# Optimization experiments

Hardware: AMD Instinct MI355X
Metric: run time of the kernel (lower is better)

The kernel has to match this reference:

```python
import jax, jax.numpy as jnp
import numpy as np

B, S, H = 32, 2048, 1024

def setup_inputs() -> dict:
    key = jax.random.key(0)
    ks = jax.random.split(key, 8)
    scale = 1.0 / np.sqrt(H)
    return {
        "query": jax.random.normal(ks[0], (B, H), jnp.float32),
        "keys": jax.random.normal(ks[1], (B, S, H), jnp.float32),
        "Wa_w": jax.random.uniform(ks[2], (H, H), jnp.float32, -scale, scale),
        "Wa_b": jax.random.uniform(ks[3], (H,), jnp.float32, -scale, scale),
        "Ua_w": jax.random.uniform(ks[4], (H, H), jnp.float32, -scale, scale),
        "Ua_b": jax.random.uniform(ks[5], (H,), jnp.float32, -scale, scale),
        "Va_w": jax.random.uniform(ks[6], (1, H), jnp.float32, -scale, scale),
        "Va_b": jax.random.uniform(ks[7], (1,), jnp.float32, -scale, scale),
    }

def reference(query, keys, Wa_w, Wa_b, Ua_w, Ua_b, Va_w, Va_b):
    # q_proj: [B, H]; k_proj: [B, S, H]  (torch Linear: x @ W^T + b)
    q_proj = query @ Wa_w.T + Wa_b
    k_proj = jnp.einsum("bsh,gh->bsg", keys, Ua_w) + Ua_b
    # scores: [B, S, 1] via thin Va projection of tanh-combined features
    scores = jnp.tanh(q_proj[:, None, :] + k_proj) @ Va_w.T + Va_b
    weights = jax.nn.softmax(scores, axis=1)            # [B, S, 1]
    context = jnp.einsum("bsx,bsh->bxh", weights, keys)  # [B, 1, H]
    return context, weights[:, :, 0]
```

## Files before the change

### kernel.cpp

```cpp
#include <hip/hip_runtime.h>
#include <hip/hip_bf16.h>
#include <stdint.h>

#define B_ 32
#define S_ 2048
#define H_ 1024

typedef __attribute__((ext_vector_type(8))) short short8;
typedef __attribute__((ext_vector_type(4))) float floatx4;

__device__ inline unsigned short f32_bf16(float f) {
    union { float f; unsigned u; } v; v.f = f;
    unsigned u = v.u;
    u += 0x7fff + ((u >> 16) & 1);
    return (unsigned short)(u >> 16);
}
__device__ inline unsigned pack_bf2(float a, float b) {
    return (unsigned)f32_bf16(a) | ((unsigned)f32_bf16(b) << 16);
}
__device__ inline float bf_lo(unsigned u) { union { unsigned u; float f; } v; v.u = u << 16; return v.f; }
__device__ inline float bf_hi(unsigned u) { union { unsigned u; float f; } v; v.u = u & 0xffff0000u; return v.f; }

__device__ inline float tanh_fast(float x) {
    float e = __expf(2.0f * x);
    return 1.0f - 2.0f / (e + 1.0f);
}

__device__ inline void gld16(const void* g, void* l) {
    __builtin_amdgcn_global_load_lds(
        (const __attribute__((address_space(1))) unsigned int*)g,
        (__attribute__((address_space(3))) unsigned int*)l, 16, 0, 0);
}

#define KCVT_BLOCKS 32768
#define UACVT_BLOCKS 512
#define QP_BLOCKS 64
__global__ void k_prep(const float* __restrict__ keys, unsigned short* __restrict__ keysbf,
                       const float* __restrict__ ua, unsigned short* __restrict__ uab,
                       const float* __restrict__ query, const float* __restrict__ Wa_w,
                       const float* __restrict__ Wa_b, const float* __restrict__ Ua_b,
                       float* __restrict__ qsum) {
    int blk = blockIdx.x, t = threadIdx.x;
    if (blk < KCVT_BLOCKS + UACVT_BLOCKS) {
        const float* src; unsigned short* dst; size_t base;
        if (blk < KCVT_BLOCKS) { src = keys; dst = keysbf; base = (size_t)blk * 2048; }
        else { src = ua; dst = uab; base = (size_t)(blk - KCVT_BLOCKS) * 2048; }
        float4 v0 = *(const float4*)(src + base + t * 4);
        float4 v1 = *(const float4*)(src + base + 1024 + t * 4);
        *(uint2*)(dst + base + t * 4)        = make_uint2(pack_bf2(v0.x, v0.y), pack_bf2(v0.z, v0.w));
        *(uint2*)(dst + base + 1024 + t * 4) = make_uint2(pack_bf2(v1.x, v1.y), pack_bf2(v1.z, v1.w));
    } else {
        __shared__ float qs_l[32][68];
        int g0 = (blk - KCVT_BLOCKS - UACVT_BLOCKS) * 16;
        int r = t >> 4, l = t & 15;
        int g = g0 + r;
        float acc[32];
#pragma unroll
        for (int b = 0; b < 32; ++b) acc[b] = 0.0f;
        int sb = t >> 3, sc = (t & 7) * 8;
        for (int hc = 0; hc < 16; ++hc) {
            __syncthreads();
            float4 v0 = *(const float4*)(query + (size_t)sb * H_ + hc * 64 + sc);
            float4 v1 = *(const float4*)(query + (size_t)sb * H_ + hc * 64 + sc + 4);
            *(float4*)&qs_l[sb][sc]     = v0;
            *(float4*)&qs_l[sb][sc + 4] = v1;
            __syncthreads();
            float4 w = *(const float4*)(Wa_w + (size_t)g * H_ + hc * 64 + l * 4);
#pragma unroll
            for (int b = 0; b < 32; ++b) {
                float4 q4 = *(const float4*)&qs_l[b][l * 4];
                acc[b] += w.x * q4.x + w.y * q4.y + w.z * q4.z + w.w * q4.w;
            }
        }
#pragma unroll
        for (int b = 0; b < 32; ++b) {
            float a = acc[b];
            a += __shfl_xor(a, 1); a += __shfl_xor(a, 2);
            a += __shfl_xor(a, 4); a += __shfl_xor(a, 8);
            acc[b] = a;
        }
        if (l == 0) {
            float bias = Wa_b[g] + Ua_b[g];
#pragma unroll
            for (int b = 0; b < 32; ++b) qsum[b * H_ + g] = acc[b] + bias;
        }
    }
}

#define BM 128
#define BN 128
#define BK 64

__global__ __launch_bounds__(256, 4) void k_scores(
    const unsigned short* __restrict__ keysbf, const unsigned short* __restrict__ uab,
    const float* __restrict__ qsum, const float* __restrict__ va,
    float* __restrict__ scores_p)
{
    __shared__ unsigned short Al[BM * BK];
    __shared__ unsigned short Bl[BN * BK];

    int bx = blockIdx.x;
    int x  = bx & 7;
    int i  = bx >> 3;
    int tile_m = x * 64 + (i >> 3);
    int nc     = i & 7;
    int m_base = tile_m * BM;
    int b      = m_base >> 11;
    int g0     = nc * BN;

    int tid = threadIdx.x;
    int wid = tid >> 6, lane = tid & 63;
    int wm = wid >> 1, wn = wid & 1;
    int q = lane >> 4, cn = lane & 15;

    int rl8 = lane >> 3;
    int gcg = (lane & 7) ^ rl8;
    const unsigned short* pA[4];
    const unsigned short* pB[4];
    unsigned short* lA[4];
    unsigned short* lB[4];
#pragma unroll
    for (int j = 0; j < 4; ++j) {
        int row = wid * 32 + j * 8 + rl8;
        pA[j] = keysbf + (size_t)(m_base + row) * H_ + gcg * 8;
        pB[j] = uab    + (size_t)(g0     + row) * H_ + gcg * 8;
        lA[j] = &Al[(wid * 32 + j * 8) * BK];
        lB[j] = &Bl[(wid * 32 + j * 8) * BK];
    }

    int aoff[2][4], boff[2][4];
#pragma unroll
    for (int kk = 0; kk < 2; ++kk)
#pragma unroll
        for (int ii = 0; ii < 4; ++ii) {
            int r  = wm * 64 + ii * 16 + cn;
            aoff[kk][ii] = r * BK + ((kk * 4 + q) ^ (r & 7)) * 8;
            int rb = wn * 64 + ii * 16 + cn;
            boff[kk][ii] = rb * BK + ((kk * 4 + q) ^ (rb & 7)) * 8;
        }

    floatx4 acc[4][4];
#pragma unroll
    for (int ii = 0; ii < 4; ++ii)
#pragma unroll
        for (int jj = 0; jj < 4; ++jj)
            acc[ii][jj] = (floatx4)(0.0f);

    for (int kc = 0; kc < H_ / BK; ++kc) {
        __syncthreads();
        int ko = kc * BK;
#pragma unroll
        for (int j = 0; j < 4; ++j) {
            gld16(pA[j] + ko, lA[j]);
            gld16(pB[j] + ko, lB[j]);
        }
        __syncthreads();
#pragma unroll
        for (int kk = 0; kk < 2; ++kk) {
            short8 af[4], bf[4];
#pragma unroll
            for (int ii = 0; ii < 4; ++ii) af[ii] = *(const short8*)&Al[aoff[kk][ii]];
#pragma unroll
            for (int jj = 0; jj < 4; ++jj) bf[jj] = *(const short8*)&Bl[boff[kk][jj]];
#pragma unroll
            for (int ii = 0; ii < 4; ++ii)
#pragma unroll
                for (int jj = 0; jj < 4; ++jj)
                    acc[ii][jj] = __builtin_amdgcn_mfma_f32_16x16x32_bf16(
                        af[ii], bf[jj], acc[ii][jj], 0, 0, 0);
        }
    }

    float qs[4], vw[4];
#pragma unroll
    for (int jj = 0; jj < 4; ++jj) {
        int g = g0 + wn * 64 + jj * 16 + cn;
        qs[jj] = qsum[b * H_ + g];
        vw[jj] = va[g];
    }
    float* slab = scores_p + (size_t)nc * (B_ * S_) + b * S_;
#pragma unroll
    for (int ii = 0; ii < 4; ++ii) {
        float rs[4] = {0.f, 0.f, 0.f, 0.f};
#pragma unroll
        for (int jj = 0; jj < 4; ++jj) {
#pragma unroll
            for (int r = 0; r < 4; ++r)
                rs[r] += vw[jj] * tanh_fast(qs[jj] + acc[ii][jj][r]);
        }
#pragma unroll
        for (int r = 0; r < 4; ++r) {
            for (int mm = 1; mm < 16; mm <<= 1)
                rs[r] += __shfl_xor(rs[r], mm);
        }
        if (cn == 0) {
            int msrow = (m_base & (S_ - 1)) + wm * 64 + ii * 16 + q * 4;
            float* sp = slab + (size_t)wn * (8 * B_ * S_) + msrow;
            sp[0] = rs[0]; sp[1] = rs[1]; sp[2] = rs[2]; sp[3] = rs[3];
        }
    }
}

__global__ void k_softmax(const float* __restrict__ scores_p, float* __restrict__ weights) {
    int b = blockIdx.x;
    int t = threadIdx.x;
    __shared__ float red[4];
    float v[8];
    float mx = -1e30f;
#pragma unroll
    for (int k = 0; k < 8; ++k) {
        int idx = b * S_ + t + k * 256;
        float s = 0.0f;
#pragma unroll
        for (int p = 0; p < 16; ++p) s += scores_p[(size_t)p * (B_ * S_) + idx];
        v[k] = s; mx = fmaxf(mx, s);
    }
    for (int mm = 1; mm < 64; mm <<= 1) mx = fmaxf(mx, __shfl_xor(mx, mm));
    if ((t & 63) == 0) red[t >> 6] = mx;
    __syncthreads();
    mx = fmaxf(fmaxf(red[0], red[1]), fmaxf(red[2], red[3]));
    float sum = 0.0f;
#pragma unroll
    for (int k = 0; k < 8; ++k) { v[k] = __expf(v[k] - mx); sum += v[k]; }
    for (int mm = 1; mm < 64; mm <<= 1) sum += __shfl_xor(sum, mm);
    __syncthreads();
    if ((t & 63) == 0) red[t >> 6] = sum;
    __syncthreads();
    sum = red[0] + red[1] + red[2] + red[3];
    float inv = 1.0f / sum;
#pragma unroll
    for (int k = 0; k < 8; ++k) weights[b * S_ + t + k * 256] = v[k] * inv;
}

__global__ void k_ctx1(const unsigned short* __restrict__ keysbf,
                       const float* __restrict__ weights, float* __restrict__ partial) {
    int blk = blockIdx.x;
    int b = blk >> 5, sc = blk & 31;
    int t = threadIdx.x;
    __shared__ float wl[64];
    if (t < 64) wl[t] = weights[b * S_ + sc * 64 + t];
    __syncthreads();
    const uint4* kp = (const uint4*)(keysbf + (size_t)(b * S_ + sc * 64) * H_);
    int col = t & 127;
    int rp  = t >> 7;
    float a0=0,a1=0,a2=0,a3=0,a4=0,a5=0,a6=0,a7=0;
#pragma unroll 8
    for (int s = rp; s < 64; s += 2) {
        uint4 v = kp[(size_t)s * 128 + col];
        float w = wl[s];
        a0 += w * bf_lo(v.x); a1 += w * bf_hi(v.x);
        a2 += w * bf_lo(v.y); a3 += w * bf_hi(v.y);
        a4 += w * bf_lo(v.z); a5 += w * bf_hi(v.z);
        a6 += w * bf_lo(v.w); a7 += w * bf_hi(v.w);
    }
    float* pp = partial + (size_t)(b * 64 + sc * 2 + rp) * H_ + col * 8;
    float4 o0 = {a0, a1, a2, a3}, o1 = {a4, a5, a6, a7};
    *(float4*)pp = o0;
    *(float4*)(pp + 4) = o1;
}

__global__ void k_ctx2(const float* __restrict__ partial, float* __restrict__ ctx) {
    int b = blockIdx.x;
    int t = threadIdx.x;
    float4 a = {0.f, 0.f, 0.f, 0.f};
#pragma unroll 8
    for (int j = 0; j < 64; ++j) {
        float4 p = *(const float4*)(partial + (size_t)(b * 64 + j) * H_ + t * 4);
        a.x += p.x; a.y += p.y; a.z += p.z; a.w += p.w;
    }
    *(float4*)(ctx + b * H_ + t * 4) = a;
}

extern "C" void kernel_launch(void* const* d_in, const int* in_sizes, int n_in,
                              void* d_out, int out_size, void* d_ws, size_t ws_size,
                              hipStream_t stream) {
    const float* query = (const float*)d_in[0];
    const float* keys  = (const float*)d_in[1];
    const float* Wa_w  = (const float*)d_in[2];
    const float* Wa_b  = (const float*)d_in[3];
    const float* Ua_w  = (const float*)d_in[4];
    const float* Ua_b  = (const float*)d_in[5];
    const float* Va_w  = (const float*)d_in[6];

    float* out     = (float*)d_out;
    float* ctx     = out;
    float* weights = out + B_ * H_;

    char* ws = (char*)d_ws;
    unsigned short* keysbf  = (unsigned short*)ws;
    unsigned short* uab     = (unsigned short*)(ws + 134217728);
    float*          qsum    = (float*)(ws + 134217728 + 2097152);
    float*          scores_p= (float*)(ws + 134217728 + 2097152 + 131072);
    float*          partial = (float*)(ws + 134217728 + 2097152 + 131072 + 4194304);

    k_prep   <<<KCVT_BLOCKS + UACVT_BLOCKS + QP_BLOCKS, 256, 0, stream>>>(
        keys, keysbf, Ua_w, uab, query, Wa_w, Wa_b, Ua_b, qsum);
    k_scores <<<4096, 256, 0, stream>>>(keysbf, uab, qsum, Va_w, scores_p);
    k_softmax<<<B_, 256, 0, stream>>>(scores_p, weights);
    k_ctx1   <<<B_ * 32, 256, 0, stream>>>(keysbf, weights, partial);
    k_ctx2   <<<B_, 256, 0, stream>>>(partial, ctx);
}
```

Baseline: 589.9 us.

## Restructure score GEMM into 256x256 tiles with double-buffered, split-phase LDS pipeline

The score GEMM moves from 128x128 tiles with 256 threads to 256x256 tiles with 512 threads and 8 waves. LDS is double-buffered and global-to-LDS loads are issued in quarter-tile stages, interleaved with MFMA phases through explicit vmcnt waits, barriers and setprio. The aim is to overlap memory traffic with matrix math and raise data reuse per loaded byte. In exchange it uses more LDS and registers per block, lowers occupancy, and the hand-tuned waitcnt schedule is fragile.

```diff
diff --git a/kernel.cpp b/kernel.cpp
--- a/kernel.cpp
+++ b/kernel.cpp
@@ -87,89 +87,143 @@
     }
 }
 
-#define BM 128
-#define BN 128
+#define BM 256
+#define BN 256
 #define BK 64
 
-__global__ __launch_bounds__(256, 4) void k_scores(
+#define VMCNT(S) asm volatile("s_waitcnt vmcnt(" S ")" ::: "memory")
+
+#define STAGE_A(SB, h, KO) do {                                                       \
+    gld16(pAj[0] + (h) * 64 * H_ + (KO), &Al[(SB) * 16384 + (h) * 8192 + sA]);        \
+    gld16(pAj[1] + (h) * 64 * H_ + (KO), &Al[(SB) * 16384 + (h) * 8192 + sA + 512]);  \
+} while (0)
+#define STAGE_B(SB, h, KO) do {                                                       \
+    gld16(pBj[0] + (h) * 32 * H_ + (KO), &Bl[(SB) * 16384 + (h) * 8192 + sA]);        \
+    gld16(pBj[1] + (h) * 32 * H_ + (KO), &Bl[(SB) * 16384 + (h) * 8192 + sA + 512]);  \
+} while (0)
+
+#define MFMA_BF16 __builtin_amdgcn_mfma_f32_16x16x32_bf16
+
+#define STEP(RB, SB, KO, W1, W2, W3, DOST) do {                                        \
+                        \
+    if (DOST) STAGE_A(SB, 0, KO);                                                      \
+    VMCNT(W1);                                                                         \
+    __builtin_amdgcn_s_barrier();                                                      \
+    _Pragma("unroll") for (int ii_ = 0; ii_ < 4; ++ii_) {                              \
+        af[ii_][0] = *(const short8*)&Al[(RB) + arA + ii_ * 1024 + cs0];               \
+        af[ii_][1] = *(const short8*)&Al[(RB) + arA + ii_ * 1024 + cs1]; }             \
+    _Pragma("unroll") for (int jj_ = 0; jj_ < 2; ++jj_) {                              \
+        bfa[jj_][0] = *(const short8*)&Bl[(RB) + brB + jj_ * 1024 + cs0];              \
+        bfa[jj_][1] = *(const short8*)&Bl[(RB) + brB + jj_ * 1024 + cs1]; }            \
+    __builtin_amdgcn_s_setprio(1);                                                     \
+    _Pragma("unroll") for (int ii_ = 0; ii_ < 4; ++ii_)                                \
+    _Pragma("unroll") for (int jj_ = 0; jj_ < 2; ++jj_) {                              \
+        acc[ii_][jj_] = MFMA_BF16(af[ii_][0], bfa[jj_][0], acc[ii_][jj_], 0, 0, 0);    \
+        acc[ii_][jj_] = MFMA_BF16(af[ii_][1], bfa[jj_][1], acc[ii_][jj_], 0, 0, 0); }  \
+    __builtin_amdgcn_s_setprio(0);                                                     \
+    __builtin_amdgcn_s_barrier();                                                      \
+                           \
+    if (DOST) STAGE_B(SB, 0, KO);                                                      \
+    VMCNT(W2);                                                                         \
+    __builtin_amdgcn_s_barrier();                                                      \
+    _Pragma("unroll") for (int jj_ = 0; jj_ < 2; ++jj_) {                              \
+        bfb[jj_][0] = *(const short8*)&Bl[(RB) + 8192 + brB + jj_ * 1024 + cs0];       \
+        bfb[jj_][1] = *(const short8*)&Bl[(RB) + 8192 + brB + jj_ * 1024 + cs1]; }     \
+    __builtin_amdgcn_s_setprio(1);                                                     \
+    _Pragma("unroll") for (int ii_ = 0; ii_ < 4; ++ii_)                                \
+    _Pragma("unroll") for (int jj_ = 0; jj_ < 2; ++jj_) {                              \
+        acc[ii_][jj_ + 2] = MFMA_BF16(af[ii_][0], bfb[jj_][0], acc[ii_][jj_ + 2], 0, 0, 0); \
+        acc[ii_][jj_ + 2] = MFMA_BF16(af[ii_][1], bfb[jj_][1], acc[ii_][jj_ + 2], 0, 0, 0); } \
+    __builtin_amdgcn_s_setprio(0);                                                     \
+    __builtin_amdgcn_s_barrier();                                                      \
+                           \
+    if (DOST) STAGE_B(SB, 1, KO);                                                      \
+    VMCNT(W3);                                                                         \
+    __builtin_amdgcn_s_barrier();                                                      \
+    _Pragma("unroll") for (int ii_ = 0; ii_ < 4; ++ii_) {                              \
+        af[ii_][0] = *(const short8*)&Al[(RB) + 8192 + arA + ii_ * 1024 + cs0];        \
+        af[ii_][1] = *(const short8*)&Al[(RB) + 8192 + arA + ii_ * 1024 + cs1]; }      \
+    __builtin_amdgcn_s_setprio(1);                                                     \
+    _Pragma("unroll") for (int ii_ = 0; ii_ < 4; ++ii_)                                \
+    _Pragma("unroll") for (int jj_ = 0; jj_ < 2; ++jj_) {                              \
+        acc[ii_ + 4][jj_] = MFMA_BF16(af[ii_][0], bfa[jj_][0], acc[ii_ + 4][jj_], 0, 0, 0); \
+        acc[ii_ + 4][jj_] = MFMA_BF16(af[ii_][1], bfa[jj_][1], acc[ii_ + 4][jj_], 0, 0, 0); } \
+    __builtin_amdgcn_s_setprio(0);                                                     \
+    __builtin_amdgcn_s_barrier();                                                      \
+                        \
+    if (DOST) STAGE_A(SB, 1, KO);                                                      \
+    __builtin_amdgcn_s_setprio(1);                                                     \
+    _Pragma("unroll") for (int ii_ = 0; ii_ < 4; ++ii_)                                \
+    _Pragma("unroll") for (int jj_ = 0; jj_ < 2; ++jj_) {                              \
+        acc[ii_ + 4][jj_ + 2] = MFMA_BF16(af[ii_][0], bfb[jj_][0], acc[ii_ + 4][jj_ + 2], 0, 0, 0); \
+        acc[ii_ + 4][jj_ + 2] = MFMA_BF16(af[ii_][1], bfb[jj_][1], acc[ii_ + 4][jj_ + 2], 0, 0, 0); } \
+    __builtin_amdgcn_s_setprio(0);                                                     \
+    __builtin_amdgcn_s_barrier();                                                      \
+} while (0)
+
+__global__ __launch_bounds__(512, 2) void k_scores(
     const unsigned short* __restrict__ keysbf, const unsigned short* __restrict__ uab,
     const float* __restrict__ qsum, const float* __restrict__ va,
     float* __restrict__ scores_p)
 {
-    __shared__ unsigned short Al[BM * BK];
-    __shared__ unsigned short Bl[BN * BK];
+    __shared__ unsigned short Al[32768];
+    __shared__ unsigned short Bl[32768];
 
     int bx = blockIdx.x;
     int x  = bx & 7;
     int i  = bx >> 3;
-    int tile_m = x * 64 + (i >> 3);
-    int nc     = i & 7;
+    int tile_m = x * 32 + (i >> 2);
+    int nc     = i & 3;
     int m_base = tile_m * BM;
     int b      = m_base >> 11;
     int g0     = nc * BN;
 
     int tid = threadIdx.x;
     int wid = tid >> 6, lane = tid & 63;
-    int wm = wid >> 1, wn = wid & 1;
+    int wm = wid >> 2, wn = wid & 3;
     int q = lane >> 4, cn = lane & 15;
+    int c7 = cn & 7;
 
     int rl8 = lane >> 3;
     int gcg = (lane & 7) ^ rl8;
-    const unsigned short* pA[4];
-    const unsigned short* pB[4];
-    unsigned short* lA[4];
-    unsigned short* lB[4];
-#pragma unroll
-    for (int j = 0; j < 4; ++j) {
-        int row = wid * 32 + j * 8 + rl8;
-        pA[j] = keysbf + (size_t)(m_base + row) * H_ + gcg * 8;
-        pB[j] = uab    + (size_t)(g0     + row) * H_ + gcg * 8;
-        lA[j] = &Al[(wid * 32 + j * 8) * BK];
-        lB[j] = &Bl[(wid * 32 + j * 8) * BK];
-    }
-
-    int aoff[2][4], boff[2][4];
-#pragma unroll
-    for (int kk = 0; kk < 2; ++kk)
-#pragma unroll
-        for (int ii = 0; ii < 4; ++ii) {
-            int r  = wm * 64 + ii * 16 + cn;
-            aoff[kk][ii] = r * BK + ((kk * 4 + q) ^ (r & 7)) * 8;
-            int rb = wn * 64 + ii * 16 + cn;
-            boff[kk][ii] = rb * BK + ((kk * 4 + q) ^ (rb & 7)) * 8;
-        }
-
-    floatx4 acc[4][4];
-#pragma unroll
-    for (int ii = 0; ii < 4; ++ii)
+    int ch0 = wid * 2;
+    const unsigned short* pAj[2];
+    const unsigned short* pBj[2];
+#pragma unroll
+    for (int j = 0; j < 2; ++j) {
+        int hlrow = (ch0 + j) * 8 + rl8;
+        pAj[j] = keysbf + (size_t)(m_base + (hlrow >> 6) * 128 + (hlrow & 63)) * H_ + gcg * 8;
+        pBj[j] = uab    + (size_t)(g0 + (hlrow >> 5) * 64 + (hlrow & 31)) * H_ + gcg * 8;
+    }
+    int sA = ch0 * 512;
+
+    int arA = wm * 4096 + cn * 64;
+    int brB = wn * 2048 + cn * 64;
+    int cs0 = (q ^ c7) * 8;
+    int cs1 = ((4 + q) ^ c7) * 8;
+
+    floatx4 acc[8][4];
+#pragma unroll
+    for (int ii = 0; ii < 8; ++ii)
 #pragma unroll
         for (int jj = 0; jj < 4; ++jj)
             acc[ii][jj] = (floatx4)(0.0f);
 
-    for (int kc = 0; kc < H_ / BK; ++kc) {
-        __syncthreads();
-        int ko = kc * BK;
-#pragma unroll
-        for (int j = 0; j < 4; ++j) {
-            gld16(pA[j] + ko, lA[j]);
-            gld16(pB[j] + ko, lB[j]);
-        }
-        __syncthreads();
-#pragma unroll
-        for (int kk = 0; kk < 2; ++kk) {
-            short8 af[4], bf[4];
-#pragma unroll
-            for (int ii = 0; ii < 4; ++ii) af[ii] = *(const short8*)&Al[aoff[kk][ii]];
-#pragma unroll
-            for (int jj = 0; jj < 4; ++jj) bf[jj] = *(const short8*)&Bl[boff[kk][jj]];
-#pragma unroll
-            for (int ii = 0; ii < 4; ++ii)
-#pragma unroll
-                for (int jj = 0; jj < 4; ++jj)
-                    acc[ii][jj] = __builtin_amdgcn_mfma_f32_16x16x32_bf16(
-                        af[ii], bf[jj], acc[ii][jj], 0, 0, 0);
-        }
-    }
+    short8 af[4][2], bfa[2][2], bfb[2][2];
+
+    STAGE_A(0, 0, 0);
+    STAGE_B(0, 0, 0);
+    STAGE_B(0, 1, 0);
+    STAGE_A(0, 1, 0);
+
+#pragma unroll 1
+    for (int it = 0; it < 7; ++it) {
+        int ko = it * 128 + 64;
+        STEP(0,     1, ko,      "6", "6", "6", 1);
+        STEP(16384, 0, ko + 64, "6", "6", "6", 1);
+    }
+    STEP(0,     1, 960, "6", "6", "6", 1);
+    STEP(16384, 0, 0,   "4", "2", "0", 0);
 
     float qs[4], vw[4];
 #pragma unroll
@@ -178,9 +232,9 @@
         qs[jj] = qsum[b * H_ + g];
         vw[jj] = va[g];
     }
-    float* slab = scores_p + (size_t)nc * (B_ * S_) + b * S_;
-#pragma unroll
-    for (int ii = 0; ii < 4; ++ii) {
+    float* slab = scores_p + (size_t)(wn * 4 + nc) * (B_ * S_) + b * S_;
+#pragma unroll
+    for (int ii = 0; ii < 8; ++ii) {
         float rs[4] = {0.f, 0.f, 0.f, 0.f};
 #pragma unroll
         for (int jj = 0; jj < 4; ++jj) {
@@ -190,12 +244,12 @@
         }
 #pragma unroll
         for (int r = 0; r < 4; ++r) {
-            for (int mm = 1; mm < 16; mm <<= 1)
-                rs[r] += __shfl_xor(rs[r], mm);
+            rs[r] += __shfl_xor(rs[r], 1); rs[r] += __shfl_xor(rs[r], 2);
+            rs[r] += __shfl_xor(rs[r], 4); rs[r] += __shfl_xor(rs[r], 8);
         }
         if (cn == 0) {
-            int msrow = (m_base & (S_ - 1)) + wm * 64 + ii * 16 + q * 4;
-            float* sp = slab + (size_t)wn * (8 * B_ * S_) + msrow;
+            int msrow = (m_base & (S_ - 1)) + wm * 128 + ii * 16 + q * 4;
+            float* sp = slab + msrow;
             sp[0] = rs[0]; sp[1] = rs[1]; sp[2] = rs[2]; sp[3] = rs[3];
         }
     }
@@ -295,7 +349,7 @@
 
     k_prep   <<<KCVT_BLOCKS + UACVT_BLOCKS + QP_BLOCKS, 256, 0, stream>>>(
         keys, keysbf, Ua_w, uab, query, Wa_w, Wa_b, Ua_b, qsum);
-    k_scores <<<4096, 256, 0, stream>>>(keysbf, uab, qsum, Va_w, scores_p);
+    k_scores <<<1024, 512, 0, stream>>>(keysbf, uab, qsum, Va_w, scores_p);
     k_softmax<<<B_, 256, 0, stream>>>(scores_p, weights);
     k_ctx1   <<<B_ * 32, 256, 0, stream>>>(keysbf, weights, partial);
     k_ctx2   <<<B_, 256, 0, stream>>>(partial, ctx);
```

New measurement: 597.5 us. About the same (+1.3%).

## Fuse context reduction into one kernel and widen softmax blocks

Applied to the files above, without the earlier changes.

Replaces the two-pass context computation (per-chunk partials in global memory, then a separate reduction kernel) with a single kernel where each block covers one batch and a 128-column slice over all 2048 rows, reducing in shared memory. This removes the partial buffer round trip and one launch. Softmax now uses 1024 threads per block instead of 256, so each thread handles fewer elements. The trade-off is less parallelism for ctx (256 blocks instead of 1024), with longer serial loops per thread.

```diff
diff --git a/kernel.cpp b/kernel.cpp
--- a/kernel.cpp
+++ b/kernel.cpp
@@ -204,71 +204,67 @@
 __global__ void k_softmax(const float* __restrict__ scores_p, float* __restrict__ weights) {
     int b = blockIdx.x;
     int t = threadIdx.x;
-    __shared__ float red[4];
-    float v[8];
-    float mx = -1e30f;
-#pragma unroll
-    for (int k = 0; k < 8; ++k) {
-        int idx = b * S_ + t + k * 256;
+    __shared__ float redm[16];
+    __shared__ float reds[16];
+    int wv = t >> 6;
+    float v0 = 0.0f, v1 = 0.0f;
+#pragma unroll
+    for (int p = 0; p < 16; ++p) {
+        const float* sp = scores_p + (size_t)p * (B_ * S_) + b * S_;
+        v0 += sp[t];
+        v1 += sp[t + 1024];
+    }
+    float mx = fmaxf(v0, v1);
+    for (int mm = 1; mm < 64; mm <<= 1) mx = fmaxf(mx, __shfl_xor(mx, mm));
+    if ((t & 63) == 0) redm[wv] = mx;
+    __syncthreads();
+#pragma unroll
+    for (int i = 0; i < 16; ++i) mx = fmaxf(mx, redm[i]);
+    float e0 = __expf(v0 - mx), e1 = __expf(v1 - mx);
+    float sum = e0 + e1;
+    for (int mm = 1; mm < 64; mm <<= 1) sum += __shfl_xor(sum, mm);
+    if ((t & 63) == 0) reds[wv] = sum;
+    __syncthreads();
+    sum = 0.0f;
+#pragma unroll
+    for (int i = 0; i < 16; ++i) sum += reds[i];
+    float inv = 1.0f / sum;
+    weights[b * S_ + t]        = e0 * inv;
+    weights[b * S_ + t + 1024] = e1 * inv;
+}
+
+__global__ void k_ctx(const unsigned short* __restrict__ keysbf,
+                      const float* __restrict__ weights, float* __restrict__ ctx) {
+    int blk = blockIdx.x;
+    int b = blk >> 3, cc = blk & 7;
+    int t = threadIdx.x;
+    __shared__ float wl[2048];
+    __shared__ float red[32][16][9];
+#pragma unroll
+    for (int k = 0; k < 4; ++k) wl[t + k * 512] = weights[b * S_ + t + k * 512];
+    __syncthreads();
+    int c = t & 15, rg = t >> 4;
+    const uint4* kp = (const uint4*)(keysbf + (size_t)b * S_ * H_) + (size_t)cc * 16 + c;
+    float a[8] = {0.f, 0.f, 0.f, 0.f, 0.f, 0.f, 0.f, 0.f};
+#pragma unroll 4
+    for (int s = rg; s < S_; s += 32) {
+        uint4 v = kp[(size_t)s * 128];
+        float w = wl[s];
+        a[0] += w * bf_lo(v.x); a[1] += w * bf_hi(v.x);
+        a[2] += w * bf_lo(v.y); a[3] += w * bf_hi(v.y);
+        a[4] += w * bf_lo(v.z); a[5] += w * bf_hi(v.z);
+        a[6] += w * bf_lo(v.w); a[7] += w * bf_hi(v.w);
+    }
+#pragma unroll
+    for (int j = 0; j < 8; ++j) red[rg][c][j] = a[j];
+    __syncthreads();
+    if (t < 128) {
+        int c2 = t & 15, j = t >> 4;
         float s = 0.0f;
 #pragma unroll
-        for (int p = 0; p < 16; ++p) s += scores_p[(size_t)p * (B_ * S_) + idx];
-        v[k] = s; mx = fmaxf(mx, s);
-    }
-    for (int mm = 1; mm < 64; mm <<= 1) mx = fmaxf(mx, __shfl_xor(mx, mm));
-    if ((t & 63) == 0) red[t >> 6] = mx;
-    __syncthreads();
-    mx = fmaxf(fmaxf(red[0], red[1]), fmaxf(red[2], red[3]));
-    float sum = 0.0f;
-#pragma unroll
-    for (int k = 0; k < 8; ++k) { v[k] = __expf(v[k] - mx); sum += v[k]; }
-    for (int mm = 1; mm < 64; mm <<= 1) sum += __shfl_xor(sum, mm);
-    __syncthreads();
-    if ((t & 63) == 0) red[t >> 6] = sum;
-    __syncthreads();
-    sum = red[0] + red[1] + red[2] + red[3];
-    float inv = 1.0f / sum;
-#pragma unroll
-    for (int k = 0; k < 8; ++k) weights[b * S_ + t + k * 256] = v[k] * inv;
-}
-
-__global__ void k_ctx1(const unsigned short* __restrict__ keysbf,
-                       const float* __restrict__ weights, float* __restrict__ partial) {
-    int blk = blockIdx.x;
-    int b = blk >> 5, sc = blk & 31;
-    int t = threadIdx.x;
-    __shared__ float wl[64];
-    if (t < 64) wl[t] = weights[b * S_ + sc * 64 + t];
-    __syncthreads();
-    const uint4* kp = (const uint4*)(keysbf + (size_t)(b * S_ + sc * 64) * H_);
-    int col = t & 127;
-    int rp  = t >> 7;
-    float a0=0,a1=0,a2=0,a3=0,a4=0,a5=0,a6=0,a7=0;
-#pragma unroll 8
-    for (int s = rp; s < 64; s += 2) {
-        uint4 v = kp[(size_t)s * 128 + col];
-        float w = wl[s];
-        a0 += w * bf_lo(v.x); a1 += w * bf_hi(v.x);
-        a2 += w * bf_lo(v.y); a3 += w * bf_hi(v.y);
-        a4 += w * bf_lo(v.z); a5 += w * bf_hi(v.z);
-        a6 += w * bf_lo(v.w); a7 += w * bf_hi(v.w);
-    }
-    float* pp = partial + (size_t)(b * 64 + sc * 2 + rp) * H_ + col * 8;
-    float4 o0 = {a0, a1, a2, a3}, o1 = {a4, a5, a6, a7};
-    *(float4*)pp = o0;
-    *(float4*)(pp + 4) = o1;
-}
-
-__global__ void k_ctx2(const float* __restrict__ partial, float* __restrict__ ctx) {
-    int b = blockIdx.x;
-    int t = threadIdx.x;
-    float4 a = {0.f, 0.f, 0.f, 0.f};
-#pragma unroll 8
-    for (int j = 0; j < 64; ++j) {
-        float4 p = *(const float4*)(partial + (size_t)(b * 64 + j) * H_ + t * 4);
-        a.x += p.x; a.y += p.y; a.z += p.z; a.w += p.w;
-    }
-    *(float4*)(ctx + b * H_ + t * 4) = a;
+        for (int g = 0; g < 32; ++g) s += red[g][c2][j];
+        ctx[b * H_ + cc * 128 + c2 * 8 + j] = s;
+    }
 }
 
 extern "C" void kernel_launch(void* const* d_in, const int* in_sizes, int n_in,
@@ -291,12 +287,10 @@
     unsigned short* uab     = (unsigned short*)(ws + 134217728);
     float*          qsum    = (float*)(ws + 134217728 + 2097152);
     float*          scores_p= (float*)(ws + 134217728 + 2097152 + 131072);
-    float*          partial = (float*)(ws + 134217728 + 2097152 + 131072 + 4194304);
 
     k_prep   <<<KCVT_BLOCKS + UACVT_BLOCKS + QP_BLOCKS, 256, 0, stream>>>(
         keys, keysbf, Ua_w, uab, query, Wa_w, Wa_b, Ua_b, qsum);
     k_scores <<<4096, 256, 0, stream>>>(keysbf, uab, qsum, Va_w, scores_p);
-    k_softmax<<<B_, 256, 0, stream>>>(scores_p, weights);
-    k_ctx1   <<<B_ * 32, 256, 0, stream>>>(keysbf, weights, partial);
-    k_ctx2   <<<B_, 256, 0, stream>>>(partial, ctx);
-}
+    k_softmax<<<B_, 1024, 0, stream>>>(scores_p, weights);
+    k_ctx    <<<B_ * 8, 512, 0, stream>>>(keysbf, weights, ctx);
+}
```

New measurement: 584.1 us. No clear change (-1.0%).
